# Optimization experiments

Measured on AMD Instinct MI355X. Metric: run time of the kernel, lower is better.

## Reference

```python
import jax, jax.numpy as jnp
import numpy as np

HIDDEN = 256
TOPK = 16
SINK_BLOCKS = 5
TAU = 1.0
SOFT_ALPHA = 8.0
LN_EPS = 1e-5


def setup_inputs() -> dict:
    key = jax.random.key(0)
    ks = jax.random.split(key, 8)
    B, T, QD, KD, J = 2, 1024, 1024, 1024, 64
    H = HIDDEN
    H3 = 3 * H
    s = 0.02
    return {
        "Q": jax.random.normal(ks[0], (B, T, QD), dtype=jnp.float32),
        "K": jax.random.normal(ks[1], (B, J, KD), dtype=jnp.float32),
        "Wq": jax.random.normal(ks[2], (H, QD), dtype=jnp.float32) * s,
        "Wk": jax.random.normal(ks[3], (H, KD), dtype=jnp.float32) * s,
        "ln_g": jnp.ones((H3,), dtype=jnp.float32),
        "ln_b": jnp.zeros((H3,), dtype=jnp.float32),
        "Wu": jax.random.normal(ks[4], (H, H3), dtype=jnp.float32) * s,
        "bu": jnp.zeros((H,), dtype=jnp.float32),
        "Wv": jax.random.normal(ks[5], (H, H3), dtype=jnp.float32) * s,
        "bv": jnp.zeros((H,), dtype=jnp.float32),
        "Wo": jax.random.normal(ks[6], (1, H), dtype=jnp.float32) * s,
        "bo": jnp.zeros((1,), dtype=jnp.float32),
        "chunk_len": 16,
        "L_ctx": 1024,
    }


def _forward(Q, K, Wq, Wk, ln_g, ln_b, Wu, bu, Wv, bv, Wo, bo, chunk_len, L_ctx):
    B, T, _ = Q.shape
    J = K.shape[1]
    # ---- GatedScorer ----
    q = jnp.einsum('btd,hd->bth', Q, Wq)  # (B,T,H)
    k = jnp.einsum('bjd,hd->bjh', K, Wk)  # (B,J,H)
    H = q.shape[-1]
    qb = jnp.broadcast_to(q[:, :, None, :], (B, T, J, H))
    kb = jnp.broadcast_to(k[:, None, :, :], (B, T, J, H))
    x = jnp.concatenate([qb, kb, qb * kb], axis=-1)  # (B,T,J,3H)
    mu = jnp.mean(x, axis=-1, keepdims=True)
    var = jnp.mean((x - mu) ** 2, axis=-1, keepdims=True)
    x = (x - mu) / jnp.sqrt(var + LN_EPS) * ln_g + ln_b
    U = jnp.einsum('btjc,hc->btjh', x, Wu) + bu
    V = jnp.einsum('btjc,hc->btjh', x, Wv) + bv
    Z = U * jax.nn.gelu(V, approximate=False)
    logits = jnp.einsum('btjh,oh->btjo', Z, Wo)[..., 0] + bo[0]  # (B,T,J)

    # ---- top-k chunk selection (deterministic path, use_learnable_k=False) ----
    sink = int(min(max(0, SINK_BLOCKS), J))
    J_tail = J - sink
    topk_main = max(min(J, TOPK) - sink, 0)
    logits_tail = logits[..., sink:]  # (B,T,J_tail)
    causal = jnp.arange(J_tail)[None, :] <= jnp.arange(T)[:, None]  # tril(T,J_tail)
    masked = jnp.where(causal[None], logits_tail, -jnp.inf)
    _, idx_tail = jax.lax.top_k(masked, topk_main)
    idx_tail = idx_tail + sink
    sink_idx = jnp.broadcast_to(jnp.arange(sink)[None, None, :], (B, T, sink))
    idx = jnp.concatenate([sink_idx, idx_tail], axis=-1)  # (B,T,sink+topk_main)

    # ---- soft warmup weights ----
    w_soft = jax.nn.softmax(logits / TAU, axis=-1)  # (B,T,J)

    # ---- build_block_bias_from_topk ----
    num_chunks = (L_ctx + chunk_len - 1) // chunk_len
    sel = jnp.zeros((B, T, num_chunks), dtype=bool)
    sel = sel.at[jnp.arange(B)[:, None, None], jnp.arange(T)[None, :, None], idx].set(True)
    token_chunk = jnp.clip(jnp.arange(L_ctx) // chunk_len, 0, num_chunks - 1)  # (L_ctx,)
    sel_tok = jnp.take(sel, token_chunk, axis=-1)  # (B,T,L_ctx)
    per_chunk_bias = -SOFT_ALPHA * (1.0 - w_soft)  # (B,T,J)
    bias = jnp.take(per_chunk_bias, token_chunk, axis=-1)  # (B,T,L_ctx)
    bias = jnp.where(sel_tok, 0.0, bias)
    tri = jnp.arange(L_ctx)[None, :] > jnp.arange(T)[:, None]  # triu(T,L_ctx, diag=1)
    bias = jnp.where(tri[None], -jnp.inf, bias)
    return logits, bias


def reference(Q, K, Wq, Wk, ln_g, ln_b, Wu, bu, Wv, bv, Wo, bo, chunk_len, L_ctx):
    return _forward(Q, K, Wq, Wk, ln_g, ln_b, Wu, bu, Wv, bv, Wo, bo, chunk_len, L_ctx)
```

## Files before the change

### kernel.cpp

```cpp
#include <hip/hip_runtime.h>
#include <hip/hip_bf16.h>
#include <math.h>

#define H3 768

#define OFF_Q     0u
#define OFF_K     524288u
#define OFF_UVK   557056u
#define OFF_SQ    622592u
#define OFF_SQ2   624768u
#define OFF_WGU   626944u
#define OFF_WGV   627200u
#define OFF_CU    627456u
#define OFF_CV    627712u
#define OFF_Q2    627968u
#define OFF_K2    1152256u

#define BO_UVQ   0u
#define BO_WQF   1048576u
#define BO_WKF   1310720u
#define BO_BPK   1572864u
#define BO_WQBF  1703936u
#define BO_WKBF  1835008u

typedef __attribute__((ext_vector_type(8))) short bf16x8;
typedef __attribute__((ext_vector_type(4))) float f32x4;

__device__ __forceinline__ float bf2f(short s) {
    return __uint_as_float(((unsigned)(unsigned short)s) << 16);
}
union bfu { __hip_bfloat162 h; short2 s; };
__device__ __forceinline__ void split2(float a, float b, short* hi2, short* lo2) {
    bfu h; h.h = __float22bfloat162_rn(float2{a, b});
    float fa = bf2f(h.s.x), fb = bf2f(h.s.y);
    bfu l; l.h = __float22bfloat162_rn(float2{a - fa, b - fb});
    hi2[0] = h.s.x; hi2[1] = h.s.y;
    lo2[0] = l.s.x; lo2[1] = l.s.y;
}
__device__ __forceinline__ void split8(const float* v, bf16x8* vh, bf16x8* vl) {
    short h2[2], l2[2];
#pragma unroll
    for (int i = 0; i < 4; i++) {
        split2(v[2 * i], v[2 * i + 1], h2, l2);
        (*vh)[2 * i] = h2[0]; (*vh)[2 * i + 1] = h2[1];
        (*vl)[2 * i] = l2[0]; (*vl)[2 * i + 1] = l2[1];
    }
}

__device__ __forceinline__ float gelu_fast(float v) {
    float ar = v * 0.70710678118654752440f;
    float a = fabsf(ar);
    float t = __builtin_amdgcn_rcpf(fmaf(0.3275911f, a, 1.0f));
    float p = fmaf(fmaf(fmaf(fmaf(1.061405429f, t, -1.453152027f), t,
                             1.421413741f), t, -0.284496736f), t, 0.254829592f) * t;
    float e = __expf(-ar * ar);
    float er = fmaf(-p, e, 1.0f);
    er = copysignf(er, ar);
    return 0.5f * v * (1.0f + er);
}

__device__ __forceinline__ float wave_reduce_add(float v) {
#pragma unroll
    for (int off = 32; off > 0; off >>= 1) v += __shfl_xor(v, off, 64);
    return v;
}

__global__ __launch_bounds__(256) void prep(const float* __restrict__ Wq,
                                            const float* __restrict__ Wk,
                                            const float* __restrict__ Wu,
                                            const float* __restrict__ Wv,
                                            const float* __restrict__ g,
                                            const float* __restrict__ lb,
                                            const float* __restrict__ bu,
                                            const float* __restrict__ bv,
                                            float* __restrict__ ws,
                                            float* __restrict__ bsc) {
    int tid = threadIdx.x;
    int bid = blockIdx.x;
    if (bid < 64) {
        int h = bid * 4 + (tid >> 6);
        int lane = tid & 63;
        float su = 0.f, sv = 0.f, tu = 0.f, tv = 0.f;
#pragma unroll
        for (int i = 0; i < 12; i++) {
            int c = lane + 64 * i;
            float gg = g[c], bb = lb[c];
            float wu = Wu[h * H3 + c], wv = Wv[h * H3 + c];
            su += wu * gg; sv += wv * gg; tu += wu * bb; tv += wv * bb;
        }
        su = wave_reduce_add(su); sv = wave_reduce_add(sv);
        tu = wave_reduce_add(tu); tv = wave_reduce_add(tv);
        if (lane == 0) {
            ws[OFF_WGU + h] = su; ws[OFF_WGV + h] = sv;
            ws[OFF_CU + h] = tu + bu[h]; ws[OFF_CV + h] = tv + bv[h];
        }
        return;
    }
    float v8[8];
    bf16x8 vh, vl;
    if (bid < 320) {
        const float* W; bf16x8* dst;
        int idx;
        if (bid < 192) { idx = (bid - 64) * 256 + tid; W = Wq; dst = (bf16x8*)(bsc + BO_WQF); }
        else { idx = (bid - 192) * 256 + tid; W = Wk; dst = (bf16x8*)(bsc + BO_WKF); }
        int n = idx >> 7, k8 = idx & 127;
        const float* src = W + (size_t)n * 1024 + k8 * 8;
        *(float4*)&v8[0] = *(const float4*)src;
        *(float4*)&v8[4] = *(const float4*)(src + 4);
        split8(v8, &vh, &vl);
        int kc = k8 >> 2, grp = k8 & 3, lane = grp * 16 + (n & 15), ntg = n >> 4;
        size_t s0 = ((size_t)(kc * 16 + ntg) * 2) * 64 + lane;
        dst[s0] = vh; dst[s0 + 64] = vl;
        return;
    }
    int idx, c0;
    bf16x8* dst;
    int n;
    if (bid < 384) {
        idx = (bid - 320) * 256 + tid;
        n = idx >> 5; c0 = (idx & 31) * 8;
        dst = (bf16x8*)(bsc + BO_WQBF);
    } else if (bid < 448) {
        idx = (bid - 384) * 256 + tid;
        n = idx >> 5; c0 = 256 + (idx & 31) * 8;
        dst = (bf16x8*)(bsc + BO_WKBF);
    } else {
        idx = (bid - 448) * 256 + tid;
        n = idx >> 5; c0 = 512 + (idx & 31) * 8;
        dst = (bf16x8*)(bsc + BO_BPK);
    }
    int h, uv;
    if (bid < 448) { uv = (n < 256) ? 0 : 1; h = (n < 256) ? n : n - 256; }
    else {
        int ntg0 = n >> 4, cc = n & 15;
        uv = ntg0 & 1;
        h = ((ntg0 >> 3) << 6) | (((ntg0 >> 1) & 3) << 4) | cc;
    }
    const float* W = uv ? Wv : Wu;
#pragma unroll
    for (int i = 0; i < 8; i++) v8[i] = W[(size_t)h * H3 + c0 + i] * g[c0 + i];
    split8(v8, &vh, &vl);
    int k8 = (c0 & 255) >> 3;
    int kc = k8 >> 2, grp = k8 & 3, lane = grp * 16 + (n & 15), ntg = n >> 4;
    size_t s0 = ((size_t)(kc * 32 + ntg) * 2) * 64 + lane;
    dst[s0] = vh; dst[s0 + 64] = vl;
}

__global__ __launch_bounds__(256) void proj_mfma(const float* __restrict__ Q,
                                                 const float* __restrict__ Kin,
                                                 const float* __restrict__ bsc,
                                                 float* __restrict__ ws) {
    __shared__ __align__(16) short Ah[2][32 * 40], Al[2][32 * 40];
    int tid = threadIdx.x, bx = blockIdx.x, by = blockIdx.y, ks = blockIdx.z;
    const float* A; float* C; const bf16x8* BF;
    if (by < 64) {
        A = Q + (size_t)by * 32 * 1024;
        C = ws + (ks ? OFF_Q2 : OFF_Q) + (size_t)by * 32 * 256;
        BF = (const bf16x8*)(bsc + BO_WQF);
    } else {
        A = Kin + (size_t)(by - 64) * 32 * 1024;
        C = ws + (ks ? OFF_K2 : OFF_K) + (size_t)(by - 64) * 32 * 256;
        BF = (const bf16x8*)(bsc + BO_WKF);
    }
    int w = tid >> 6, l = tid & 63, c15 = l & 15, grp = l >> 4;
    int mt = w & 1, np = w >> 1;
    int srow = tid >> 3, scol = (tid & 7) * 4;
    const float* arow = A + (size_t)srow * 1024 + ks * 512 + scol;
    f32x4 acc[2];
    acc[0] = (f32x4){0.f, 0.f, 0.f, 0.f};
    acc[1] = (f32x4){0.f, 0.f, 0.f, 0.f};
    float4 a4 = *(const float4*)&arow[0];
    for (int kc = 0; kc < 16; kc++) {
        int pb = kc & 1;
        short h4[4], l4[4];
        split2(a4.x, a4.y, &h4[0], &l4[0]);
        split2(a4.z, a4.w, &h4[2], &l4[2]);
        int ao = srow * 40 + scol;
        *(short4*)&Ah[pb][ao] = *(short4*)&h4[0];
        *(short4*)&Al[pb][ao] = *(short4*)&l4[0];
        if (kc < 15) a4 = *(const float4*)&arow[(kc + 1) * 32];
        __syncthreads();
        int fo = (mt * 16 + c15) * 40 + grp * 8;
        bf16x8 afh = *(const bf16x8*)&Ah[pb][fo];
        bf16x8 afl = *(const bf16x8*)&Al[pb][fo];
        int kcg = ks * 16 + kc;
        bf16x8 bh[2], bl[2];
#pragma unroll
        for (int i = 0; i < 2; i++) {
            int ntg = bx * 4 + 2 * np + i;
            size_t fi = ((size_t)(kcg * 16 + ntg) * 2) * 64 + l;
            bh[i] = BF[fi]; bl[i] = BF[fi + 64];
        }
#pragma unroll
        for (int i = 0; i < 2; i++)
            acc[i] = __builtin_amdgcn_mfma_f32_16x16x32_bf16(afl, bh[i], acc[i], 0, 0, 0);
#pragma unroll
        for (int i = 0; i < 2; i++)
            acc[i] = __builtin_amdgcn_mfma_f32_16x16x32_bf16(afh, bl[i], acc[i], 0, 0, 0);
#pragma unroll
        for (int i = 0; i < 2; i++)
            acc[i] = __builtin_amdgcn_mfma_f32_16x16x32_bf16(afh, bh[i], acc[i], 0, 0, 0);
    }
#pragma unroll
    for (int r = 0; r < 4; r++) {
        int rloc = mt * 16 + grp * 4 + r;
#pragma unroll
        for (int i = 0; i < 2; i++)
            C[(size_t)rloc * 256 + bx * 64 + (2 * np + i) * 16 + c15] = acc[i][r];
    }
}

__global__ __launch_bounds__(256) void uv_mfma(float* __restrict__ ws,
                                               float* __restrict__ bsc) {
    __shared__ __align__(16) short Ah[64 * 40], Al[64 * 40];
    int tid = threadIdx.x, bx = blockIdx.x, by = blockIdx.y;
    const float* A1; const float* A2; float* C; const bf16x8* BF; int sbase;
    if (by < 32) {
        A1 = ws + OFF_Q + (size_t)by * 64 * 256;
        A2 = ws + OFF_Q2 + (size_t)by * 64 * 256;
        C = bsc + BO_UVQ + (size_t)by * 64 * 512;
        BF = (const bf16x8*)(bsc + BO_WQBF);
        sbase = by * 64;
    } else {
        A1 = ws + OFF_K + (size_t)(by - 32) * 64 * 256;
        A2 = ws + OFF_K2 + (size_t)(by - 32) * 64 * 256;
        C = ws + OFF_UVK + (size_t)(by - 32) * 64 * 512;
        BF = (const bf16x8*)(bsc + BO_WKBF);
        sbase = 2048 + (by - 32) * 64;
    }
    int w = tid >> 6, l = tid & 63, c15 = l & 15, grp = l >> 4;
    int srow = tid >> 2, scol = (tid & 3) * 8;
    f32x4 acc[4];
#pragma unroll
    for (int nt = 0; nt < 4; nt++) acc[nt] = (f32x4){0.f, 0.f, 0.f, 0.f};
    float s1 = 0.f, s2 = 0.f;
    for (int kc = 0; kc < 8; kc++) {
        float v8[8], u8[8];
        const float* src1 = &A1[(size_t)srow * 256 + kc * 32 + scol];
        const float* src2 = &A2[(size_t)srow * 256 + kc * 32 + scol];
        *(float4*)&v8[0] = *(const float4*)src1;
        *(float4*)&v8[4] = *(const float4*)(src1 + 4);
        *(float4*)&u8[0] = *(const float4*)src2;
        *(float4*)&u8[4] = *(const float4*)(src2 + 4);
#pragma unroll
        for (int i = 0; i < 8; i++) v8[i] += u8[i];
        if (bx == 0) {
#pragma unroll
            for (int i = 0; i < 8; i++) { s1 += v8[i]; s2 = fmaf(v8[i], v8[i], s2); }
        }
        bf16x8 vh, vl;
        split8(v8, &vh, &vl);
        int ao = srow * 40 + scol;
        *(bf16x8*)&Ah[ao] = vh;
        *(bf16x8*)&Al[ao] = vl;
        __syncthreads();
        int fo = (w * 16 + c15) * 40 + grp * 8;
        bf16x8 afh = *(const bf16x8*)&Ah[fo];
        bf16x8 afl = *(const bf16x8*)&Al[fo];
        bf16x8 bh[4], bl[4];
#pragma unroll
        for (int nt = 0; nt < 4; nt++) {
            int ntg = bx * 4 + nt;
            size_t fi = ((size_t)(kc * 32 + ntg) * 2) * 64 + l;
            bh[nt] = BF[fi]; bl[nt] = BF[fi + 64];
        }
#pragma unroll
        for (int nt = 0; nt < 4; nt++)
            acc[nt] = __builtin_amdgcn_mfma_f32_16x16x32_bf16(afl, bh[nt], acc[nt], 0, 0, 0);
#pragma unroll
        for (int nt = 0; nt < 4; nt++)
            acc[nt] = __builtin_amdgcn_mfma_f32_16x16x32_bf16(afh, bl[nt], acc[nt], 0, 0, 0);
#pragma unroll
        for (int nt = 0; nt < 4; nt++)
            acc[nt] = __builtin_amdgcn_mfma_f32_16x16x32_bf16(afh, bh[nt], acc[nt], 0, 0, 0);
        __syncthreads();
    }
    if (bx == 0) {
        s1 += __shfl_xor(s1, 1, 64); s1 += __shfl_xor(s1, 2, 64);
        s2 += __shfl_xor(s2, 1, 64); s2 += __shfl_xor(s2, 2, 64);
        if ((tid & 3) == 0) {
            ws[OFF_SQ + sbase + srow] = s1;
            ws[OFF_SQ2 + sbase + srow] = s2;
        }
    }
#pragma unroll
    for (int nt = 0; nt < 4; nt++)
#pragma unroll
        for (int r = 0; r < 4; r++)
            C[(size_t)(w * 16 + grp * 4 + r) * 512 + bx * 64 + nt * 16 + c15] = acc[nt][r];
}

__global__ __launch_bounds__(512, 2) void main_mfma(const float* __restrict__ ws,
                                                    const float* __restrict__ bsc,
                                                    const float* __restrict__ Wo,
                                                    const float* __restrict__ bo,
                                                    float* __restrict__ logits) {
    __shared__ float kk[256];
    __shared__ __align__(16) short Ah[8][64 * 32];
    __shared__ __align__(16) short Al[8][64 * 32];
    __shared__ float mu_s[64], inv_s[64];
    __shared__ float part_s[8][64];
    int tid = threadIdx.x;
    int bidf = blockIdx.x;
    int ti = ((bidf & 7) << 1) | ((bidf >> 3) & 1);
    int j = (bidf >> 4) & 63;
    int b = bidf >> 10;
    int t0 = ti << 6;
    int bj = (b << 6) | j;
    int rot8 = bidf & 7;
    if (tid < 256) kk[tid] = ws[OFF_K + bj * 256 + tid] + ws[OFF_K2 + bj * 256 + tid];
    int w = tid >> 6, l = tid & 63, c15 = l & 15, grp = l >> 4;
    int srow = tid >> 3, scol = (tid & 7) * 4;
    const float* qrow = ws + OFF_Q + (size_t)((b << 10) + t0 + srow) * 256;
    const float* q2row = ws + OFF_Q2 + (size_t)((b << 10) + t0 + srow) * 256;
    const bf16x8* bpk = (const bf16x8*)(bsc + BO_BPK);
    const float* UVQ = bsc + BO_UVQ;
    f32x4 acc[4][4];
#pragma unroll
    for (int mt = 0; mt < 4; mt++)
#pragma unroll
        for (int nt = 0; nt < 4; nt++) acc[mt][nt] = (f32x4){0.f, 0.f, 0.f, 0.f};
    float s1 = 0.f, s2 = 0.f;
    int ntg0 = w * 4;
    __syncthreads();
#pragma unroll
    for (int kc = 0; kc < 8; kc++) {
        float4 q4 = *(const float4*)&qrow[kc * 32 + scol];
        float4 p4 = *(const float4*)&q2row[kc * 32 + scol];
        float4 k4 = *(const float4*)&kk[kc * 32 + scol];
        float a0 = (q4.x + p4.x) * k4.x, a1 = (q4.y + p4.y) * k4.y;
        float a2 = (q4.z + p4.z) * k4.z, a3 = (q4.w + p4.w) * k4.w;
        s1 += (a0 + a1) + (a2 + a3);
        s2 = fmaf(a0, a0, s2); s2 = fmaf(a1, a1, s2);
        s2 = fmaf(a2, a2, s2); s2 = fmaf(a3, a3, s2);
        short h4[4], l4[4];
        split2(a0, a1, &h4[0], &l4[0]);
        split2(a2, a3, &h4[2], &l4[2]);
        int ao = srow * 32 + scol;
        *(short4*)&Ah[kc][ao] = *(short4*)&h4[0];
        *(short4*)&Al[kc][ao] = *(short4*)&l4[0];
    }
    s1 += __shfl_xor(s1, 1, 64); s1 += __shfl_xor(s1, 2, 64); s1 += __shfl_xor(s1, 4, 64);
    s2 += __shfl_xor(s2, 1, 64); s2 += __shfl_xor(s2, 2, 64); s2 += __shfl_xor(s2, 4, 64);
    if ((tid & 7) == 0) {
        int row = (b << 10) + t0 + srow;
        float sq = s1 + ws[OFF_SQ + row] + ws[OFF_SQ + 2048 + bj];
        float sq2 = s2 + ws[OFF_SQ2 + row] + ws[OFF_SQ2 + 2048 + bj];
        float muv = sq * (1.0f / 768.0f);
        float ex2 = sq2 * (1.0f / 768.0f);
        mu_s[srow] = muv;
        inv_s[srow] = 1.0f / sqrtf(ex2 - muv * muv + 1e-5f);
    }
    __syncthreads();
#pragma unroll
    for (int ii = 0; ii < 8; ii++) {
        int kcg = (ii + rot8) & 7;
        bf16x8 afh[4], afl[4];
#pragma unroll
        for (int mt = 0; mt < 4; mt++) {
            int ao = (mt * 16 + c15) * 32 + grp * 8;
            afh[mt] = *(const bf16x8*)&Ah[kcg][ao];
            afl[mt] = *(const bf16x8*)&Al[kcg][ao];
        }
        bf16x8 bh[4], bl[4];
#pragma unroll
        for (int nt = 0; nt < 4; nt++) {
            size_t fi = ((size_t)(kcg * 32 + ntg0 + nt) * 2) * 64 + l;
            bh[nt] = bpk[fi];
            bl[nt] = bpk[fi + 64];
        }
#pragma unroll
        for (int nt = 0; nt < 4; nt++) {
#pragma unroll
            for (int mt = 0; mt < 4; mt++)
                acc[mt][nt] = __builtin_amdgcn_mfma_f32_16x16x32_bf16(afl[mt], bh[nt], acc[mt][nt], 0, 0, 0);
#pragma unroll
            for (int mt = 0; mt < 4; mt++)
                acc[mt][nt] = __builtin_amdgcn_mfma_f32_16x16x32_bf16(afh[mt], bl[nt], acc[mt][nt], 0, 0, 0);
#pragma unroll
            for (int mt = 0; mt < 4; mt++)
                acc[mt][nt] = __builtin_amdgcn_mfma_f32_16x16x32_bf16(afh[mt], bh[nt], acc[mt][nt], 0, 0, 0);
        }
    }
    float wgu_r[2], wgv_r[2], cu_r[2], cv_r[2], wo_r[2], uk_r[2], vk_r[2];
    int h2[2];
#pragma unroll
    for (int a = 0; a < 2; a++) {
        int ntg = 4 * w + 2 * a;
        int h = ((ntg >> 3) << 6) | (((ntg >> 1) & 3) << 4) | c15;
        h2[a] = h;
        wgu_r[a] = ws[OFF_WGU + h]; wgv_r[a] = ws[OFF_WGV + h];
        cu_r[a] = ws[OFF_CU + h]; cv_r[a] = ws[OFF_CV + h];
        wo_r[a] = Wo[h];
        uk_r[a] = ws[OFF_UVK + (size_t)bj * 512 + h];
        vk_r[a] = ws[OFF_UVK + (size_t)bj * 512 + 256 + h];
    }
#pragma unroll
    for (int mt = 0; mt < 4; mt++) {
#pragma unroll
        for (int r4 = 0; r4 < 4; r4++) {
            int r = mt * 16 + grp * 4 + r4;
            int row = (b << 10) + t0 + r;
            float muv = mu_s[r], invv = inv_s[r];
            const float* uvq = UVQ + (size_t)row * 512;
            float part = 0.f;
#pragma unroll
            for (int a = 0; a < 2; a++) {
                float U = invv * (acc[mt][2 * a][r4] + uvq[h2[a]] + uk_r[a] - muv * wgu_r[a]) + cu_r[a];
                float V = invv * (acc[mt][2 * a + 1][r4] + uvq[256 + h2[a]] + vk_r[a] - muv * wgv_r[a]) + cv_r[a];
                part = fmaf(wo_r[a] * U, gelu_fast(V), part);
            }
            part += __shfl_xor(part, 1, 64);
            part += __shfl_xor(part, 2, 64);
            part += __shfl_xor(part, 4, 64);
            part += __shfl_xor(part, 8, 64);
            if (c15 == 0) part_s[w][r] = part;
        }
    }
    __syncthreads();
    if (tid < 64) {
        float v = bo[0];
#pragma unroll
        for (int ww = 0; ww < 8; ww++) v += part_s[ww][tid];
        logits[(size_t)((b << 10) + t0 + tid) * 64 + j] = v;
    }
}

__global__ __launch_bounds__(256) void topk_bias(const float* __restrict__ logits,
                                                 float* __restrict__ bias,
                                                 const int* __restrict__ p_cl,
                                                 const int* __restrict__ p_L) {
    int wv = threadIdx.x >> 6, lane = threadIdx.x & 63;
    int row = blockIdx.x * 4 + wv;
    int t = row & 1023;
    __shared__ float pcb[4][64];
    float L = logits[(size_t)row * 64 + lane];
    float mx = L;
#pragma unroll
    for (int off = 32; off > 0; off >>= 1) mx = fmaxf(mx, __shfl_xor(mx, off, 64));
    float e = expf(L - mx);
    float s = wave_reduce_add(e);
    pcb[wv][lane] = -8.0f * (1.0f - e / s);
    bool valid = (lane >= 5) && ((lane - 5) <= t);
    float val = (lane >= 5) ? (valid ? L : -INFINITY) : -INFINITY;
    int idv = (lane >= 5) ? lane : (1 << 28);
    unsigned long long selmask = 0x1Full;
    for (int it = 0; it < 11; it++) {
        float bv = val; int bi = idv;
#pragma unroll
        for (int off = 32; off > 0; off >>= 1) {
            float ov = __shfl_xor(bv, off, 64);
            int oi = __shfl_xor(bi, off, 64);
            if (ov > bv || (ov == bv && oi < bi)) { bv = ov; bi = oi; }
        }
        selmask |= 1ull << bi;
        if (lane == bi) { val = -INFINITY; idv = (1 << 27); }
    }
    int clen = p_cl[0], Lctx = p_L[0];
    int nch1 = (Lctx + clen - 1) / clen - 1;
    float* brow = bias + (size_t)row * Lctx;
    if ((Lctx & 3) == 0) {
        float4* brow4 = (float4*)brow;
        for (int q = lane; q < (Lctx >> 2); q += 64) {
            float o[4];
#pragma unroll
            for (int i = 0; i < 4; i++) {
                int ll = 4 * q + i;
                int c = min(min((unsigned)ll / (unsigned)clen, (unsigned)nch1), 63u);
                float v;
                if (ll > t) v = -1e30f;
                else if ((selmask >> c) & 1ull) v = 0.0f;
                else v = pcb[wv][c];
                o[i] = v;
            }
            brow4[q] = *(float4*)&o[0];
        }
    } else {
        for (int ll = lane; ll < Lctx; ll += 64) {
            int c = min(min((unsigned)ll / (unsigned)clen, (unsigned)nch1), 63u);
            float v;
            if (ll > t) v = -1e30f;
            else if ((selmask >> c) & 1ull) v = 0.0f;
            else v = pcb[wv][c];
            brow[ll] = v;
        }
    }
}

extern "C" void kernel_launch(void* const* d_in, const int* in_sizes, int n_in,
                              void* d_out, int out_size, void* d_ws, size_t ws_size,
                              hipStream_t stream) {
    const float* Q   = (const float*)d_in[0];
    const float* Kin = (const float*)d_in[1];
    const float* Wq  = (const float*)d_in[2];
    const float* Wk  = (const float*)d_in[3];
    const float* g   = (const float*)d_in[4];
    const float* lb  = (const float*)d_in[5];
    const float* Wu  = (const float*)d_in[6];
    const float* bu  = (const float*)d_in[7];
    const float* Wv  = (const float*)d_in[8];
    const float* bv  = (const float*)d_in[9];
    const float* Wo  = (const float*)d_in[10];
    const float* bo  = (const float*)d_in[11];
    const int* p_cl  = (const int*)d_in[12];
    const int* p_L   = (const int*)d_in[13];
    float* ws = (float*)d_ws;
    float* logits = (float*)d_out;
    float* bias = (float*)d_out + (size_t)2 * 1024 * 64;

    prep<<<512, 256, 0, stream>>>(Wq, Wk, Wu, Wv, g, lb, bu, bv, ws, bias);
    proj_mfma<<<dim3(4, 68, 2), 256, 0, stream>>>(Q, Kin, bias, ws);
    uv_mfma<<<dim3(8, 34), 256, 0, stream>>>(ws, bias);
    main_mfma<<<2048, 512, 0, stream>>>(ws, bias, Wo, bo, logits);
    topk_bias<<<512, 256, 0, stream>>>(logits, bias, p_cl, p_L);
}
```

Baseline: 254.4 us.

## Halve main_mfma block to 4 waves, each computing 8 N-tiles

Shrinks the main scoring kernel block from 512 to 256 threads, with each wave now owning 8 output column tiles instead of 4. Each A fragment loaded from LDS is reused across twice as many MFMAs, and the staging loop writes 8-wide bf16 vectors per thread. The aim is to cut LDS reads per MFMA and per-block overhead. The cost is a doubled accumulator array (128 floats per lane), which adds register pressure and may lower occupancy or cause spills, and B fragments are now loaded inside the nt loop.

Result: faster. 234.1 us (-8.0%).

```diff
diff --git a/kernel.cpp b/kernel.cpp
--- a/kernel.cpp
+++ b/kernel.cpp
@@ -290,7 +290,7 @@
             C[(size_t)(w * 16 + grp * 4 + r) * 512 + bx * 64 + nt * 16 + c15] = acc[nt][r];
 }
 
-__global__ __launch_bounds__(512, 2) void main_mfma(const float* __restrict__ ws,
+__global__ __launch_bounds__(256, 2) void main_mfma(const float* __restrict__ ws,
                                                     const float* __restrict__ bsc,
                                                     const float* __restrict__ Wo,
                                                     const float* __restrict__ bo,
@@ -299,7 +299,7 @@
     __shared__ __align__(16) short Ah[8][64 * 32];
     __shared__ __align__(16) short Al[8][64 * 32];
     __shared__ float mu_s[64], inv_s[64];
-    __shared__ float part_s[8][64];
+    __shared__ float part_s[4][64];
     int tid = threadIdx.x;
     int bidf = blockIdx.x;
     int ti = ((bidf & 7) << 1) | ((bidf >> 3) & 1);
@@ -308,41 +308,49 @@
     int t0 = ti << 6;
     int bj = (b << 6) | j;
     int rot8 = bidf & 7;
-    if (tid < 256) kk[tid] = ws[OFF_K + bj * 256 + tid] + ws[OFF_K2 + bj * 256 + tid];
+    kk[tid] = ws[OFF_K + bj * 256 + tid] + ws[OFF_K2 + bj * 256 + tid];
     int w = tid >> 6, l = tid & 63, c15 = l & 15, grp = l >> 4;
-    int srow = tid >> 3, scol = (tid & 7) * 4;
-    const float* qrow = ws + OFF_Q + (size_t)((b << 10) + t0 + srow) * 256;
-    const float* q2row = ws + OFF_Q2 + (size_t)((b << 10) + t0 + srow) * 256;
+    int srow = tid >> 2, scol = (tid & 3) * 8;
+    const float* qrow = ws + OFF_Q + (size_t)((b << 10) + t0 + srow) * 256 + scol;
+    const float* q2row = ws + OFF_Q2 + (size_t)((b << 10) + t0 + srow) * 256 + scol;
     const bf16x8* bpk = (const bf16x8*)(bsc + BO_BPK);
     const float* UVQ = bsc + BO_UVQ;
-    f32x4 acc[4][4];
+    f32x4 acc[4][8];
 #pragma unroll
     for (int mt = 0; mt < 4; mt++)
 #pragma unroll
-        for (int nt = 0; nt < 4; nt++) acc[mt][nt] = (f32x4){0.f, 0.f, 0.f, 0.f};
+        for (int nt = 0; nt < 8; nt++) acc[mt][nt] = (f32x4){0.f, 0.f, 0.f, 0.f};
     float s1 = 0.f, s2 = 0.f;
-    int ntg0 = w * 4;
+    int ntg0 = w * 8;
     __syncthreads();
 #pragma unroll
     for (int kc = 0; kc < 8; kc++) {
-        float4 q4 = *(const float4*)&qrow[kc * 32 + scol];
-        float4 p4 = *(const float4*)&q2row[kc * 32 + scol];
-        float4 k4 = *(const float4*)&kk[kc * 32 + scol];
-        float a0 = (q4.x + p4.x) * k4.x, a1 = (q4.y + p4.y) * k4.y;
-        float a2 = (q4.z + p4.z) * k4.z, a3 = (q4.w + p4.w) * k4.w;
-        s1 += (a0 + a1) + (a2 + a3);
-        s2 = fmaf(a0, a0, s2); s2 = fmaf(a1, a1, s2);
-        s2 = fmaf(a2, a2, s2); s2 = fmaf(a3, a3, s2);
-        short h4[4], l4[4];
-        split2(a0, a1, &h4[0], &l4[0]);
-        split2(a2, a3, &h4[2], &l4[2]);
+        float q8[8], p8[8], kv[8];
+        *(float4*)&q8[0] = *(const float4*)&qrow[kc * 32];
+        *(float4*)&q8[4] = *(const float4*)&qrow[kc * 32 + 4];
+        *(float4*)&p8[0] = *(const float4*)&q2row[kc * 32];
+        *(float4*)&p8[4] = *(const float4*)&q2row[kc * 32 + 4];
+        *(float4*)&kv[0] = *(const float4*)&kk[kc * 32 + scol];
+        *(float4*)&kv[4] = *(const float4*)&kk[kc * 32 + scol + 4];
+        bf16x8 vh, vl;
+        short htmp[2], ltmp[2];
+#pragma unroll
+        for (int i = 0; i < 4; i++) {
+            float a = (q8[2 * i] + p8[2 * i]) * kv[2 * i];
+            float c = (q8[2 * i + 1] + p8[2 * i + 1]) * kv[2 * i + 1];
+            s1 += a + c;
+            s2 = fmaf(a, a, s2); s2 = fmaf(c, c, s2);
+            split2(a, c, htmp, ltmp);
+            vh[2 * i] = htmp[0]; vh[2 * i + 1] = htmp[1];
+            vl[2 * i] = ltmp[0]; vl[2 * i + 1] = ltmp[1];
+        }
         int ao = srow * 32 + scol;
-        *(short4*)&Ah[kc][ao] = *(short4*)&h4[0];
-        *(short4*)&Al[kc][ao] = *(short4*)&l4[0];
-    }
-    s1 += __shfl_xor(s1, 1, 64); s1 += __shfl_xor(s1, 2, 64); s1 += __shfl_xor(s1, 4, 64);
-    s2 += __shfl_xor(s2, 1, 64); s2 += __shfl_xor(s2, 2, 64); s2 += __shfl_xor(s2, 4, 64);
-    if ((tid & 7) == 0) {
+        *(bf16x8*)&Ah[kc][ao] = vh;
+        *(bf16x8*)&Al[kc][ao] = vl;
+    }
+    s1 += __shfl_xor(s1, 1, 64); s1 += __shfl_xor(s1, 2, 64);
+    s2 += __shfl_xor(s2, 1, 64); s2 += __shfl_xor(s2, 2, 64);
+    if ((tid & 3) == 0) {
         int row = (b << 10) + t0 + srow;
         float sq = s1 + ws[OFF_SQ + row] + ws[OFF_SQ + 2048 + bj];
         float sq2 = s2 + ws[OFF_SQ2 + row] + ws[OFF_SQ2 + 2048 + bj];
@@ -362,33 +370,28 @@
             afh[mt] = *(const bf16x8*)&Ah[kcg][ao];
             afl[mt] = *(const bf16x8*)&Al[kcg][ao];
         }
-        bf16x8 bh[4], bl[4];
-#pragma unroll
-        for (int nt = 0; nt < 4; nt++) {
-            size_t fi = ((size_t)(kcg * 32 + ntg0 + nt) * 2) * 64 + l;
-            bh[nt] = bpk[fi];
-            bl[nt] = bpk[fi + 64];
-        }
-#pragma unroll
-        for (int nt = 0; nt < 4; nt++) {
+        const bf16x8* bpc = bpk + ((size_t)(kcg * 32 + ntg0) * 2) * 64 + l;
+#pragma unroll
+        for (int nt = 0; nt < 8; nt++) {
+            bf16x8 bh = bpc[(size_t)nt * 128];
+            bf16x8 bl = bpc[(size_t)nt * 128 + 64];
 #pragma unroll
             for (int mt = 0; mt < 4; mt++)
-                acc[mt][nt] = __builtin_amdgcn_mfma_f32_16x16x32_bf16(afl[mt], bh[nt], acc[mt][nt], 0, 0, 0);
+                acc[mt][nt] = __builtin_amdgcn_mfma_f32_16x16x32_bf16(afl[mt], bh, acc[mt][nt], 0, 0, 0);
 #pragma unroll
             for (int mt = 0; mt < 4; mt++)
-                acc[mt][nt] = __builtin_amdgcn_mfma_f32_16x16x32_bf16(afh[mt], bl[nt], acc[mt][nt], 0, 0, 0);
+                acc[mt][nt] = __builtin_amdgcn_mfma_f32_16x16x32_bf16(afh[mt], bl, acc[mt][nt], 0, 0, 0);
 #pragma unroll
             for (int mt = 0; mt < 4; mt++)
-                acc[mt][nt] = __builtin_amdgcn_mfma_f32_16x16x32_bf16(afh[mt], bh[nt], acc[mt][nt], 0, 0, 0);
-        }
-    }
-    float wgu_r[2], wgv_r[2], cu_r[2], cv_r[2], wo_r[2], uk_r[2], vk_r[2];
-    int h2[2];
-#pragma unroll
-    for (int a = 0; a < 2; a++) {
-        int ntg = 4 * w + 2 * a;
-        int h = ((ntg >> 3) << 6) | (((ntg >> 1) & 3) << 4) | c15;
-        h2[a] = h;
+                acc[mt][nt] = __builtin_amdgcn_mfma_f32_16x16x32_bf16(afh[mt], bh, acc[mt][nt], 0, 0, 0);
+        }
+    }
+    float wgu_r[4], wgv_r[4], cu_r[4], cv_r[4], wo_r[4], uk_r[4], vk_r[4];
+    int h4[4];
+#pragma unroll
+    for (int a = 0; a < 4; a++) {
+        int h = (w << 6) | (a << 4) | c15;
+        h4[a] = h;
         wgu_r[a] = ws[OFF_WGU + h]; wgv_r[a] = ws[OFF_WGV + h];
         cu_r[a] = ws[OFF_CU + h]; cv_r[a] = ws[OFF_CV + h];
         wo_r[a] = Wo[h];
@@ -405,9 +408,9 @@
             const float* uvq = UVQ + (size_t)row * 512;
             float part = 0.f;
 #pragma unroll
-            for (int a = 0; a < 2; a++) {
-                float U = invv * (acc[mt][2 * a][r4] + uvq[h2[a]] + uk_r[a] - muv * wgu_r[a]) + cu_r[a];
-                float V = invv * (acc[mt][2 * a + 1][r4] + uvq[256 + h2[a]] + vk_r[a] - muv * wgv_r[a]) + cv_r[a];
+            for (int a = 0; a < 4; a++) {
+                float U = invv * (acc[mt][2 * a][r4] + uvq[h4[a]] + uk_r[a] - muv * wgu_r[a]) + cu_r[a];
+                float V = invv * (acc[mt][2 * a + 1][r4] + uvq[256 + h4[a]] + vk_r[a] - muv * wgv_r[a]) + cv_r[a];
                 part = fmaf(wo_r[a] * U, gelu_fast(V), part);
             }
             part += __shfl_xor(part, 1, 64);
@@ -419,9 +422,7 @@
     }
     __syncthreads();
     if (tid < 64) {
-        float v = bo[0];
-#pragma unroll
-        for (int ww = 0; ww < 8; ww++) v += part_s[ww][tid];
+        float v = bo[0] + part_s[0][tid] + part_s[1][tid] + part_s[2][tid] + part_s[3][tid];
         logits[(size_t)((b << 10) + t0 + tid) * 64 + j] = v;
     }
 }
@@ -511,6 +512,6 @@
     prep<<<512, 256, 0, stream>>>(Wq, Wk, Wu, Wv, g, lb, bu, bv, ws, bias);
     proj_mfma<<<dim3(4, 68, 2), 256, 0, stream>>>(Q, Kin, bias, ws);
     uv_mfma<<<dim3(8, 34), 256, 0, stream>>>(ws, bias);
-    main_mfma<<<2048, 512, 0, stream>>>(ws, bias, Wo, bo, logits);
+    main_mfma<<<2048, 256, 0, stream>>>(ws, bias, Wo, bo, logits);
     topk_bias<<<512, 256, 0, stream>>>(logits, bias, p_cl, p_L);
 }
```
